# Kernel tuning notes

Measured on AMD Instinct MI355X. Metric: run time of the kernel, lower is better.

## Reference

```python
import jax, jax.numpy as jnp
import numpy as np

N, E = 100000, 1600000
IN_DIM, HID, NCLS = 64, 128, 18
BATCH, K = 8, 5000


def setup_inputs() -> dict:
    key = jax.random.key(0)
    ks = jax.random.split(key, 9)
    features = jax.random.normal(ks[0], (N, IN_DIM), dtype=jnp.float32)
    src = jax.random.randint(ks[1], (E,), 0, N, dtype=jnp.int32)
    dst = jax.random.randint(ks[2], (E,), 0, N, dtype=jnp.int32)
    def glorot(k, shape):
        lim = float(np.sqrt(6.0 / (shape[0] + shape[1])))
        return jax.random.uniform(k, shape, jnp.float32, -lim, lim)
    W1 = glorot(ks[3], (IN_DIM, HID)); b1 = jnp.zeros((HID,), jnp.float32)
    W2 = glorot(ks[4], (HID, HID));    b2 = jnp.zeros((HID,), jnp.float32)
    W3 = glorot(ks[5], (K * HID, NCLS)); b3 = jnp.zeros((NCLS,), jnp.float32)
    return {"features": features, "src": src, "dst": dst,
            "W1": W1, "b1": b1, "W2": W2, "b2": b2, "W3": W3, "b3": b3}


def reference(features, src, dst, W1, b1, W2, b2, W3, b3):
    n = features.shape[0]
    ones = jnp.ones(src.shape[0], features.dtype)
    out_deg = jax.ops.segment_sum(ones, src, num_segments=n)
    in_deg = jax.ops.segment_sum(ones, dst, num_segments=n)
    norm_src = jnp.clip(out_deg, 1.0) ** -0.5  # DGL norm='both'
    norm_dst = jnp.clip(in_deg, 1.0) ** -0.5

    def gconv(x, W, b, act):
        h = (x @ W) * norm_src[:, None]          # transform then normalize src
        agg = jax.ops.segment_sum(h[src], dst, num_segments=n)  # gather+scatter-add
        agg = agg * norm_dst[:, None] + b
        return jax.nn.relu(agg) if act else agg

    h = gconv(features, W1, b1, True)   # [N, HID]
    h = gconv(h, W2, b2, True)          # [N, HID]

    # global_sort_pool: equal-sized graphs of N//BATCH nodes, top-K by last channel
    n_per = n // BATCH
    hb = h.reshape(BATCH, n_per, HID)
    _, idx = jax.lax.top_k(hb[..., -1], K)                  # [B, K] descending
    topk = jnp.take_along_axis(hb, idx[..., None], axis=1)  # [B, K, HID]
    pooled = topk.reshape(BATCH, K * HID)

    return pooled @ W3 + b3  # [B, NCLS]
```

## Files before the change

### kernel.cpp

```cpp
#include <hip/hip_runtime.h>
#include <cstdint>
#include <cstddef>

#define N_NODES 100000
#define N_EDGES 1600000
#define IN_DIM  64
#define HID     128
#define NCLS    18
#define BATCH   8
#define TOPK    5000
#define NPER    12500
#define SORTN   16384
#define SORTC   2048

#define BSHIFT  9
#define BNODES  (1 << BSHIFT)
#define NBUCK   ((N_NODES + BNODES - 1) / BNODES)
#define CHUNK   8192


__global__ __launch_bounds__(256) void k_bcount(const int* __restrict__ src,
                                                const int* __restrict__ dst,
                                                int* __restrict__ bcntS,
                                                int* __restrict__ bcntD) {
    __shared__ int cs[NBUCK], cd[NBUCK];
    for (int b = threadIdx.x; b < NBUCK; b += 256) { cs[b] = 0; cd[b] = 0; }
    __syncthreads();
    const int base = blockIdx.x * CHUNK;
    const int end  = min(base + CHUNK, N_EDGES);
    for (int e = base + threadIdx.x; e < end; e += 256) {
        atomicAdd(&cs[src[e] >> BSHIFT], 1);
        atomicAdd(&cd[dst[e] >> BSHIFT], 1);
    }
    __syncthreads();
    for (int b = threadIdx.x; b < NBUCK; b += 256) {
        if (cs[b]) atomicAdd(&bcntS[b], cs[b]);
        if (cd[b]) atomicAdd(&bcntD[b], cd[b]);
    }
}

__global__ void k_bscan(const int* __restrict__ bcntS, const int* __restrict__ bcntD,
                        int* __restrict__ baseS, int* __restrict__ baseD,
                        int* __restrict__ curS, int* __restrict__ curD) {
    if (threadIdx.x == 0 && blockIdx.x == 0) {
        int rs = 0, rd = 0;
        for (int b = 0; b < NBUCK; ++b) {
            baseS[b] = rs; curS[b] = rs; rs += bcntS[b];
            baseD[b] = rd; curD[b] = rd; rd += bcntD[b];
        }
        baseS[NBUCK] = rs; baseD[NBUCK] = rd;
    }
}


__global__ __launch_bounds__(256) void k_bin(const int* __restrict__ src,
                                             const int* __restrict__ dst,
                                             int* __restrict__ cursorD,
                                             unsigned* __restrict__ binbuf) {
    __shared__ int cnt[NBUCK];
    __shared__ int gbase[NBUCK];
    __shared__ int cnt2[NBUCK];
    const int base = blockIdx.x * CHUNK;
    const int end  = min(base + CHUNK, N_EDGES);
    for (int b = threadIdx.x; b < NBUCK; b += 256) { cnt[b] = 0; cnt2[b] = 0; }
    __syncthreads();
    for (int e = base + threadIdx.x; e < end; e += 256)
        atomicAdd(&cnt[dst[e] >> BSHIFT], 1);
    __syncthreads();
    for (int b = threadIdx.x; b < NBUCK; b += 256)
        if (cnt[b] > 0) gbase[b] = atomicAdd(&cursorD[b], cnt[b]);
    __syncthreads();
    for (int e = base + threadIdx.x; e < end; e += 256) {
        int d = dst[e];
        int b = d >> BSHIFT;
        int off = atomicAdd(&cnt2[b], 1);
        unsigned packed = ((unsigned)(d & (BNODES - 1)) << 17) | (unsigned)src[e];
        binbuf[gbase[b] + off] = packed;
    }
}

__global__ __launch_bounds__(256) void k_bin_src(const int* __restrict__ src,
                                                 int* __restrict__ cursorS,
                                                 unsigned* __restrict__ sbin) {
    __shared__ int cnt[NBUCK];
    __shared__ int gbase[NBUCK];
    __shared__ int cnt2[NBUCK];
    const int base = blockIdx.x * CHUNK;
    const int end  = min(base + CHUNK, N_EDGES);
    for (int b = threadIdx.x; b < NBUCK; b += 256) { cnt[b] = 0; cnt2[b] = 0; }
    __syncthreads();
    for (int e = base + threadIdx.x; e < end; e += 256)
        atomicAdd(&cnt[src[e] >> BSHIFT], 1);
    __syncthreads();
    for (int b = threadIdx.x; b < NBUCK; b += 256)
        if (cnt[b] > 0) gbase[b] = atomicAdd(&cursorS[b], cnt[b]);
    __syncthreads();
    for (int e = base + threadIdx.x; e < end; e += 256) {
        int s = src[e];
        int b = s >> BSHIFT;
        int off = atomicAdd(&cnt2[b], 1);
        sbin[gbase[b] + off] = (unsigned)(s & (BNODES - 1));
    }
}


__global__ __launch_bounds__(256) void k_histS(const unsigned* __restrict__ sbin,
                                               const int* __restrict__ baseS,
                                               float* __restrict__ normS) {
    __shared__ int cnt[BNODES];
    for (int t = threadIdx.x; t < BNODES; t += 256) cnt[t] = 0;
    __syncthreads();
    const int beg = baseS[blockIdx.x], end = baseS[blockIdx.x + 1];
    for (int e = beg + threadIdx.x; e < end; e += 256)
        atomicAdd(&cnt[sbin[e]], 1);
    __syncthreads();
    const int nodeBase = blockIdx.x << BSHIFT;
    for (int t = threadIdx.x; t < BNODES; t += 256) {
        int node = nodeBase + t;
        if (node < N_NODES)
            normS[node] = 1.0f / sqrtf((float)max(cnt[t], 1));
    }
}

__global__ __launch_bounds__(256) void k_histD_scatter(const unsigned* __restrict__ binbuf,
                                                       const int* __restrict__ baseD,
                                                       float* __restrict__ normD,
                                                       int* __restrict__ row_ptr,
                                                       int* __restrict__ ssrc) {
    __shared__ int cnt[BNODES];
    __shared__ int tmp[BNODES];
    for (int t = threadIdx.x; t < BNODES; t += 256) cnt[t] = 0;
    __syncthreads();
    const int beg = baseD[blockIdx.x], end = baseD[blockIdx.x + 1];
    for (int e = beg + threadIdx.x; e < end; e += 256)
        atomicAdd(&cnt[binbuf[e] >> 17], 1);
    __syncthreads();
    const int nodeBase = blockIdx.x << BSHIFT;
    for (int t = threadIdx.x; t < BNODES; t += 256) {
        int node = nodeBase + t;
        if (node < N_NODES)
            normD[node] = 1.0f / sqrtf((float)max(cnt[t], 1));
    }
    for (int s = 1; s < BNODES; s <<= 1) {
        for (int t = threadIdx.x; t < BNODES; t += 256)
            tmp[t] = (t >= s) ? cnt[t - s] + cnt[t] : cnt[t];
        __syncthreads();
        for (int t = threadIdx.x; t < BNODES; t += 256) cnt[t] = tmp[t];
        __syncthreads();
    }
    for (int t = threadIdx.x; t < BNODES; t += 256) {
        int b = beg + ((t == 0) ? 0 : cnt[t - 1]);
        tmp[t] = b;
        int node = nodeBase + t;
        if (node < N_NODES) row_ptr[node] = b;
    }
    if (blockIdx.x == 0 && threadIdx.x == 0) row_ptr[N_NODES] = N_EDGES;
    __syncthreads();
    for (int e = beg + threadIdx.x; e < end; e += 256) {
        unsigned v = binbuf[e];
        int pos = atomicAdd(&tmp[v >> 17], 1);
        ssrc[pos] = (int)(v & 0x1FFFFu);
    }
}


#define BMT 64
#define BKT 32

template<int KDIM>
__global__ __launch_bounds__(256) void k_gemm_rt(const float* __restrict__ X,
                                                 const float* __restrict__ W,
                                                 const float* __restrict__ normS,
                                                 float* __restrict__ out) {
    __shared__ float xs[BMT][BKT + 4];
    __shared__ float ws[BKT * HID];

    const int tid = threadIdx.x;
    const int tx = tid & 31;
    const int ty = tid >> 5;
    const int col0 = tx * 4;
    const int row0 = ty * 8;
    const int rt = blockIdx.x * BMT;

    float acc[8][4];
    #pragma unroll
    for (int r = 0; r < 8; ++r)
        #pragma unroll
        for (int c = 0; c < 4; ++c) acc[r][c] = 0.f;

    for (int k0 = 0; k0 < KDIM; k0 += BKT) {
        __syncthreads();
        {
            const float4* wsrc = (const float4*)(W + (size_t)k0 * HID);
            #pragma unroll
            for (int i = tid; i < BKT * HID / 4; i += 256)
                ((float4*)ws)[i] = wsrc[i];
        }
        {
            #pragma unroll
            for (int i = tid; i < BMT * BKT / 4; i += 256) {
                int row = i >> 3;
                int kq  = i & 7;
                int gr  = rt + row;
                float4 v = make_float4(0.f, 0.f, 0.f, 0.f);
                if (gr < N_NODES)
                    v = *(const float4*)(X + (size_t)gr * KDIM + k0 + kq * 4);
                *(float4*)&xs[row][kq * 4] = v;
            }
        }
        __syncthreads();

        #pragma unroll 4
        for (int k = 0; k < BKT; ++k) {
            float4 b = *(const float4*)&ws[k * HID + col0];
            float a[8];
            #pragma unroll
            for (int r = 0; r < 8; ++r) a[r] = xs[row0 + r][k];
            #pragma unroll
            for (int r = 0; r < 8; ++r) {
                acc[r][0] += a[r] * b.x;
                acc[r][1] += a[r] * b.y;
                acc[r][2] += a[r] * b.z;
                acc[r][3] += a[r] * b.w;
            }
        }
    }

    #pragma unroll
    for (int r = 0; r < 8; ++r) {
        int gr = rt + row0 + r;
        if (gr < N_NODES) {
            float s = normS[gr];
            float4 o = make_float4(acc[r][0] * s, acc[r][1] * s, acc[r][2] * s, acc[r][3] * s);
            *(float4*)(out + (size_t)gr * HID + col0) = o;
        }
    }
}


#define ACC4(A, V) { A.x += V.x; A.y += V.y; A.z += V.z; A.w += V.w; }

__global__ __launch_bounds__(256) void k_agg(const float* __restrict__ hs,
                                             const int* __restrict__ row_ptr,
                                             const int* __restrict__ ssrc,
                                             const float* __restrict__ normD,
                                             const float* __restrict__ bias,
                                             float* __restrict__ out,
                                             float* __restrict__ keys) {
    const int node = blockIdx.x * 8 + (threadIdx.x >> 5);
    const int lane = threadIdx.x & 31;
    if (node >= N_NODES) return;
    const int beg = row_ptr[node], end = row_ptr[node + 1];
    const float4* __restrict__ hv = (const float4*)hs;
    float4 acc = make_float4(0.f, 0.f, 0.f, 0.f);
    int e = beg;
    for (; e + 8 <= end; e += 8) {
        int s0 = ssrc[e + 0], s1 = ssrc[e + 1], s2 = ssrc[e + 2], s3 = ssrc[e + 3];
        int s4 = ssrc[e + 4], s5 = ssrc[e + 5], s6 = ssrc[e + 6], s7 = ssrc[e + 7];
        float4 v0 = hv[(size_t)s0 * 32 + lane];
        float4 v1 = hv[(size_t)s1 * 32 + lane];
        float4 v2 = hv[(size_t)s2 * 32 + lane];
        float4 v3 = hv[(size_t)s3 * 32 + lane];
        float4 v4 = hv[(size_t)s4 * 32 + lane];
        float4 v5 = hv[(size_t)s5 * 32 + lane];
        float4 v6 = hv[(size_t)s6 * 32 + lane];
        float4 v7 = hv[(size_t)s7 * 32 + lane];
        ACC4(acc, v0); ACC4(acc, v1); ACC4(acc, v2); ACC4(acc, v3);
        ACC4(acc, v4); ACC4(acc, v5); ACC4(acc, v6); ACC4(acc, v7);
    }
    if (e + 4 <= end) {
        int s0 = ssrc[e + 0], s1 = ssrc[e + 1], s2 = ssrc[e + 2], s3 = ssrc[e + 3];
        float4 v0 = hv[(size_t)s0 * 32 + lane];
        float4 v1 = hv[(size_t)s1 * 32 + lane];
        float4 v2 = hv[(size_t)s2 * 32 + lane];
        float4 v3 = hv[(size_t)s3 * 32 + lane];
        ACC4(acc, v0); ACC4(acc, v1); ACC4(acc, v2); ACC4(acc, v3);
        e += 4;
    }
    for (; e < end; ++e) {
        float4 v0 = hv[(size_t)ssrc[e] * 32 + lane];
        ACC4(acc, v0);
    }
    float nrm = normD[node];
    float4 bb = *(const float4*)(bias + lane * 4);
    float4 o;
    o.x = fmaxf(acc.x * nrm + bb.x, 0.f);
    o.y = fmaxf(acc.y * nrm + bb.y, 0.f);
    o.z = fmaxf(acc.z * nrm + bb.z, 0.f);
    o.w = fmaxf(acc.w * nrm + bb.w, 0.f);
    *(float4*)(out + (size_t)node * HID + lane * 4) = o;
    if (keys != nullptr && lane == 31) keys[node] = o.w;
}


__global__ __launch_bounds__(256) void k_sort_init(const float* __restrict__ keys,
                                                   unsigned long long* __restrict__ arr) {
    int i = blockIdx.x * 256 + threadIdx.x;
    if (i >= BATCH * SORTN) return;
    int g = i >> 14;
    int l = i & (SORTN - 1);
    unsigned long long c;
    if (l < NPER) {
        unsigned u = __float_as_uint(keys[g * NPER + l]);
        unsigned s = (u & 0x80000000u) ? ~u : (u | 0x80000000u);
        unsigned d = ~s;
        c = ((unsigned long long)d << 32) | (unsigned)l;
    } else {
        c = 0xFFFFFFFFFFFFFFFFull;
    }
    arr[i] = c;
}

__global__ __launch_bounds__(1024) void k_sort_local_full(unsigned long long* __restrict__ arr) {
    __shared__ unsigned long long lds[SORTC];
    const int base  = blockIdx.x * SORTC;
    const int gbase = base & (SORTN - 1);
    lds[threadIdx.x]        = arr[base + threadIdx.x];
    lds[threadIdx.x + 1024] = arr[base + threadIdx.x + 1024];
    __syncthreads();
    for (int k = 2; k <= SORTC; k <<= 1) {
        for (int j = k >> 1; j > 0; j >>= 1) {
            int t = threadIdx.x;
            int i = ((t & ~(j - 1)) << 1) | (t & (j - 1));
            bool up = (((gbase + i) & k) == 0);
            unsigned long long a = lds[i], b = lds[i + j];
            if ((a > b) == up) { lds[i] = b; lds[i + j] = a; }
            __syncthreads();
        }
    }
    arr[base + threadIdx.x]        = lds[threadIdx.x];
    arr[base + threadIdx.x + 1024] = lds[threadIdx.x + 1024];
}

__global__ __launch_bounds__(256) void k_sort_global(unsigned long long* __restrict__ arr,
                                                     int k, int j) {
    int tg = blockIdx.x * 256 + threadIdx.x;
    if (tg >= BATCH * (SORTN / 2)) return;
    int g = tg >> 13;
    int t = tg & (SORTN / 2 - 1);
    int i = ((t & ~(j - 1)) << 1) | (t & (j - 1));
    bool up = ((i & k) == 0);
    unsigned long long* p = arr + (size_t)g * SORTN;
    unsigned long long a = p[i], b = p[i + j];
    if ((a > b) == up) { p[i] = b; p[i + j] = a; }
}

__global__ __launch_bounds__(1024) void k_sort_local_tail(unsigned long long* __restrict__ arr,
                                                          int k) {
    __shared__ unsigned long long lds[SORTC];
    const int base  = blockIdx.x * SORTC;
    const int gbase = base & (SORTN - 1);
    lds[threadIdx.x]        = arr[base + threadIdx.x];
    lds[threadIdx.x + 1024] = arr[base + threadIdx.x + 1024];
    __syncthreads();
    for (int j = SORTC >> 1; j > 0; j >>= 1) {
        int t = threadIdx.x;
        int i = ((t & ~(j - 1)) << 1) | (t & (j - 1));
        bool up = (((gbase + i) & k) == 0);
        unsigned long long a = lds[i], b = lds[i + j];
        if ((a > b) == up) { lds[i] = b; lds[i + j] = a; }
        __syncthreads();
    }
    arr[base + threadIdx.x]        = lds[threadIdx.x];
    arr[base + threadIdx.x + 1024] = lds[threadIdx.x + 1024];
}

__global__ __launch_bounds__(256) void k_sort_emit(const unsigned long long* __restrict__ arr,
                                                   int* __restrict__ topk_idx) {
    int i = blockIdx.x * 256 + threadIdx.x;
    if (i >= BATCH * TOPK) return;
    int b = i / TOPK;
    int k = i - b * TOPK;
    topk_idx[i] = (int)(arr[(size_t)b * SORTN + k] & 0xFFFFFFFFull);
}


__global__ void k_outinit(const float* __restrict__ b3, float* __restrict__ out) {
    int i = threadIdx.x;
    if (i < BATCH * NCLS) out[i] = b3[i % NCLS];
}

#define KPB 100

__global__ __launch_bounds__(128) void k_final(const float* __restrict__ h2,
                                               const int* __restrict__ topk_idx,
                                               const float* __restrict__ W3,
                                               float* __restrict__ out) {
    __shared__ float red[128 * NCLS];
    const int b = blockIdx.x / (TOPK / KPB);
    const int chunk = blockIdx.x % (TOPK / KPB);
    const int j = threadIdx.x;
    float acc[NCLS];
    #pragma unroll
    for (int c = 0; c < NCLS; ++c) acc[c] = 0.f;
    const int k0 = chunk * KPB;
    for (int k = k0; k < k0 + KPB; ++k) {
        int node = b * NPER + topk_idx[b * TOPK + k];
        float h = h2[(size_t)node * HID + j];
        const float* wrow = W3 + (size_t)(k * HID + j) * NCLS;
        #pragma unroll
        for (int c = 0; c < NCLS; ++c) acc[c] += h * wrow[c];
    }
    #pragma unroll
    for (int c = 0; c < NCLS; ++c) red[j * NCLS + c] = acc[c];
    __syncthreads();
    for (int s = 64; s > 0; s >>= 1) {
        if (j < s) {
            #pragma unroll
            for (int c = 0; c < NCLS; ++c) red[j * NCLS + c] += red[(j + s) * NCLS + c];
        }
        __syncthreads();
    }
    if (j < NCLS) atomicAdd(&out[b * NCLS + j], red[j]);
}


extern "C" void kernel_launch(void* const* d_in, const int* in_sizes, int n_in,
                              void* d_out, int out_size, void* d_ws, size_t ws_size,
                              hipStream_t stream) {
    const float* features = (const float*)d_in[0];
    const int*   src      = (const int*)d_in[1];
    const int*   dst      = (const int*)d_in[2];
    const float* W1       = (const float*)d_in[3];
    const float* b1       = (const float*)d_in[4];
    const float* W2       = (const float*)d_in[5];
    const float* b2       = (const float*)d_in[6];
    const float* W3       = (const float*)d_in[7];
    const float* b3       = (const float*)d_in[8];
    float* out = (float*)d_out;

    char* p = (char*)d_ws;
    auto carve = [&](size_t bytes) -> void* {
        void* r = (void*)p;
        p += (bytes + 511) & ~(size_t)511;
        return r;
    };
    float* normS     = (float*)carve((size_t)N_NODES * 4);
    float* normD     = (float*)carve((size_t)N_NODES * 4);
    int*   row_ptr   = (int*)carve((size_t)(N_NODES + 1) * 4);
    int*   bcntS     = (int*)carve((size_t)NBUCK * 4);
    int*   bcntD     = (int*)carve((size_t)NBUCK * 4);
    int*   baseS     = (int*)carve((size_t)(NBUCK + 1) * 4);
    int*   baseD     = (int*)carve((size_t)(NBUCK + 1) * 4);
    int*   curS      = (int*)carve((size_t)NBUCK * 4);
    int*   curD      = (int*)carve((size_t)NBUCK * 4);
    int*   ssrc      = (int*)carve((size_t)N_EDGES * 4);
    unsigned* binbuf = (unsigned*)carve((size_t)N_EDGES * 4);
    unsigned* sbin   = (unsigned*)carve((size_t)N_EDGES * 4);
    float* keys      = (float*)carve((size_t)N_NODES * 4);
    int*   topk_idx  = (int*)carve((size_t)BATCH * TOPK * 4);
    unsigned long long* sortbuf = (unsigned long long*)carve((size_t)BATCH * SORTN * 8);
    float* bufA      = (float*)carve((size_t)N_NODES * HID * 4);
    float* bufB      = (float*)carve((size_t)N_NODES * HID * 4);

    const int GB = (N_NODES + BMT - 1) / BMT;
    const int BB = (N_EDGES + CHUNK - 1) / CHUNK;

    hipMemsetAsync(bcntS, 0, (size_t)NBUCK * 4, stream);
    hipMemsetAsync(bcntD, 0, (size_t)NBUCK * 4, stream);

    k_bcount<<<BB, 256, 0, stream>>>(src, dst, bcntS, bcntD);
    k_bscan<<<1, 64, 0, stream>>>(bcntS, bcntD, baseS, baseD, curS, curD);
    k_bin<<<BB, 256, 0, stream>>>(src, dst, curD, binbuf);
    k_bin_src<<<BB, 256, 0, stream>>>(src, curS, sbin);
    k_histS<<<NBUCK, 256, 0, stream>>>(sbin, baseS, normS);
    k_histD_scatter<<<NBUCK, 256, 0, stream>>>(binbuf, baseD, normD, row_ptr, ssrc);

    k_gemm_rt<IN_DIM><<<GB, 256, 0, stream>>>(features, W1, normS, bufA);
    k_agg<<<(N_NODES + 7) / 8, 256, 0, stream>>>(bufA, row_ptr, ssrc, normD, b1, bufB, nullptr);
    k_gemm_rt<HID><<<GB, 256, 0, stream>>>(bufB, W2, normS, bufA);
    k_agg<<<(N_NODES + 7) / 8, 256, 0, stream>>>(bufA, row_ptr, ssrc, normD, b2, bufB, keys);

    const int NCHUNK = BATCH * SORTN / SORTC;
    const int GCE    = (BATCH * (SORTN / 2) + 255) / 256;
    k_sort_init<<<(BATCH * SORTN + 255) / 256, 256, 0, stream>>>(keys, sortbuf);
    k_sort_local_full<<<NCHUNK, 1024, 0, stream>>>(sortbuf);
    k_sort_global<<<GCE, 256, 0, stream>>>(sortbuf, 4096, 2048);
    k_sort_local_tail<<<NCHUNK, 1024, 0, stream>>>(sortbuf, 4096);
    k_sort_global<<<GCE, 256, 0, stream>>>(sortbuf, 8192, 4096);
    k_sort_global<<<GCE, 256, 0, stream>>>(sortbuf, 8192, 2048);
    k_sort_local_tail<<<NCHUNK, 1024, 0, stream>>>(sortbuf, 8192);
    k_sort_global<<<GCE, 256, 0, stream>>>(sortbuf, 16384, 8192);
    k_sort_global<<<GCE, 256, 0, stream>>>(sortbuf, 16384, 4096);
    k_sort_global<<<GCE, 256, 0, stream>>>(sortbuf, 16384, 2048);
    k_sort_local_tail<<<NCHUNK, 1024, 0, stream>>>(sortbuf, 16384);
    k_sort_emit<<<(BATCH * TOPK + 255) / 256, 256, 0, stream>>>(sortbuf, topk_idx);

    k_outinit<<<1, 256, 0, stream>>>(b3, out);
    k_final<<<BATCH * (TOPK / KPB), 128, 0, stream>>>(bufB, topk_idx, W3, out);
}
```

Baseline: 650.1 us.

## Aggregate before transform in first layer and fuse normalization/bias/ReLU into GEMM epilogue

Reorders the GCN layers as aggregate-then-transform. Layer 1 now gathers 64-wide input features, scaling each by the source norm, before the GEMM, which halves the gather traffic for that layer. The destination norm, bias, ReLU, next-layer source norm and top-k key extraction all move into the GEMM epilogue, so the aggregation kernels become plain gather-sums. The cost is an extra normS gather per edge in the first aggregation, a new 64-wide intermediate buffer, and a shorter unroll (4 instead of 8) in the 128-wide aggregation.

```diff
diff --git a/kernel.cpp b/kernel.cpp
--- a/kernel.cpp
+++ b/kernel.cpp
@@ -164,13 +164,78 @@
 }
 
 
+__global__ __launch_bounds__(256) void k_agg64(const float* __restrict__ hs,
+                                               const int* __restrict__ row_ptr,
+                                               const int* __restrict__ ssrc,
+                                               const float* __restrict__ normS,
+                                               float* __restrict__ out) {
+    const int node = blockIdx.x * 16 + (threadIdx.x >> 4);
+    const int lane = threadIdx.x & 15;
+    if (node >= N_NODES) return;
+    const int beg = row_ptr[node], end = row_ptr[node + 1];
+    const float4* __restrict__ hv = (const float4*)hs;
+    float4 acc = make_float4(0.f, 0.f, 0.f, 0.f);
+    int e = beg;
+    for (; e + 4 <= end; e += 4) {
+        int s0 = ssrc[e + 0], s1 = ssrc[e + 1], s2 = ssrc[e + 2], s3 = ssrc[e + 3];
+        float n0 = normS[s0], n1 = normS[s1], n2 = normS[s2], n3 = normS[s3];
+        float4 v0 = hv[(size_t)s0 * 16 + lane];
+        float4 v1 = hv[(size_t)s1 * 16 + lane];
+        float4 v2 = hv[(size_t)s2 * 16 + lane];
+        float4 v3 = hv[(size_t)s3 * 16 + lane];
+        acc.x += v0.x * n0; acc.y += v0.y * n0; acc.z += v0.z * n0; acc.w += v0.w * n0;
+        acc.x += v1.x * n1; acc.y += v1.y * n1; acc.z += v1.z * n1; acc.w += v1.w * n1;
+        acc.x += v2.x * n2; acc.y += v2.y * n2; acc.z += v2.z * n2; acc.w += v2.w * n2;
+        acc.x += v3.x * n3; acc.y += v3.y * n3; acc.z += v3.z * n3; acc.w += v3.w * n3;
+    }
+    for (; e < end; ++e) {
+        int s0 = ssrc[e];
+        float n0 = normS[s0];
+        float4 v0 = hv[(size_t)s0 * 16 + lane];
+        acc.x += v0.x * n0; acc.y += v0.y * n0; acc.z += v0.z * n0; acc.w += v0.w * n0;
+    }
+    *(float4*)(out + (size_t)node * IN_DIM + lane * 4) = acc;
+}
+
+#define ACC4(A, V) { A.x += V.x; A.y += V.y; A.z += V.z; A.w += V.w; }
+
+__global__ __launch_bounds__(256) void k_agg128(const float* __restrict__ hs,
+                                                const int* __restrict__ row_ptr,
+                                                const int* __restrict__ ssrc,
+                                                float* __restrict__ out) {
+    const int node = blockIdx.x * 8 + (threadIdx.x >> 5);
+    const int lane = threadIdx.x & 31;
+    if (node >= N_NODES) return;
+    const int beg = row_ptr[node], end = row_ptr[node + 1];
+    const float4* __restrict__ hv = (const float4*)hs;
+    float4 acc = make_float4(0.f, 0.f, 0.f, 0.f);
+    int e = beg;
+    for (; e + 4 <= end; e += 4) {
+        int s0 = ssrc[e + 0], s1 = ssrc[e + 1], s2 = ssrc[e + 2], s3 = ssrc[e + 3];
+        float4 v0 = hv[(size_t)s0 * 32 + lane];
+        float4 v1 = hv[(size_t)s1 * 32 + lane];
+        float4 v2 = hv[(size_t)s2 * 32 + lane];
+        float4 v3 = hv[(size_t)s3 * 32 + lane];
+        ACC4(acc, v0); ACC4(acc, v1); ACC4(acc, v2); ACC4(acc, v3);
+    }
+    for (; e < end; ++e) {
+        float4 v0 = hv[(size_t)ssrc[e] * 32 + lane];
+        ACC4(acc, v0);
+    }
+    *(float4*)(out + (size_t)node * HID + lane * 4) = acc;
+}
+
+
 #define BMT 64
 #define BKT 32
 
-template<int KDIM>
+template<int KDIM, bool POST, bool KEYS>
 __global__ __launch_bounds__(256) void k_gemm_rt(const float* __restrict__ X,
                                                  const float* __restrict__ W,
+                                                 const float* __restrict__ normD,
+                                                 const float* __restrict__ bias,
                                                  const float* __restrict__ normS,
+                                                 float* __restrict__ keys,
                                                  float* __restrict__ out) {
     __shared__ float xs[BMT][BKT + 4];
     __shared__ float ws[BKT * HID];
@@ -226,70 +291,25 @@
         }
     }
 
+    const float4 bb = *(const float4*)(bias + col0);
     #pragma unroll
     for (int r = 0; r < 8; ++r) {
         int gr = rt + row0 + r;
         if (gr < N_NODES) {
-            float s = normS[gr];
-            float4 o = make_float4(acc[r][0] * s, acc[r][1] * s, acc[r][2] * s, acc[r][3] * s);
+            float nd = normD[gr];
+            float4 o;
+            o.x = fmaxf(acc[r][0] * nd + bb.x, 0.f);
+            o.y = fmaxf(acc[r][1] * nd + bb.y, 0.f);
+            o.z = fmaxf(acc[r][2] * nd + bb.z, 0.f);
+            o.w = fmaxf(acc[r][3] * nd + bb.w, 0.f);
+            if (KEYS && col0 == 124) keys[gr] = o.w;
+            if (POST) {
+                float ns = normS[gr];
+                o.x *= ns; o.y *= ns; o.z *= ns; o.w *= ns;
+            }
             *(float4*)(out + (size_t)gr * HID + col0) = o;
         }
     }
-}
-
-
-#define ACC4(A, V) { A.x += V.x; A.y += V.y; A.z += V.z; A.w += V.w; }
-
-__global__ __launch_bounds__(256) void k_agg(const float* __restrict__ hs,
-                                             const int* __restrict__ row_ptr,
-                                             const int* __restrict__ ssrc,
-                                             const float* __restrict__ normD,
-                                             const float* __restrict__ bias,
-                                             float* __restrict__ out,
-                                             float* __restrict__ keys) {
-    const int node = blockIdx.x * 8 + (threadIdx.x >> 5);
-    const int lane = threadIdx.x & 31;
-    if (node >= N_NODES) return;
-    const int beg = row_ptr[node], end = row_ptr[node + 1];
-    const float4* __restrict__ hv = (const float4*)hs;
-    float4 acc = make_float4(0.f, 0.f, 0.f, 0.f);
-    int e = beg;
-    for (; e + 8 <= end; e += 8) {
-        int s0 = ssrc[e + 0], s1 = ssrc[e + 1], s2 = ssrc[e + 2], s3 = ssrc[e + 3];
-        int s4 = ssrc[e + 4], s5 = ssrc[e + 5], s6 = ssrc[e + 6], s7 = ssrc[e + 7];
-        float4 v0 = hv[(size_t)s0 * 32 + lane];
-        float4 v1 = hv[(size_t)s1 * 32 + lane];
-        float4 v2 = hv[(size_t)s2 * 32 + lane];
-        float4 v3 = hv[(size_t)s3 * 32 + lane];
-        float4 v4 = hv[(size_t)s4 * 32 + lane];
-        float4 v5 = hv[(size_t)s5 * 32 + lane];
-        float4 v6 = hv[(size_t)s6 * 32 + lane];
-        float4 v7 = hv[(size_t)s7 * 32 + lane];
-        ACC4(acc, v0); ACC4(acc, v1); ACC4(acc, v2); ACC4(acc, v3);
-        ACC4(acc, v4); ACC4(acc, v5); ACC4(acc, v6); ACC4(acc, v7);
-    }
-    if (e + 4 <= end) {
-        int s0 = ssrc[e + 0], s1 = ssrc[e + 1], s2 = ssrc[e + 2], s3 = ssrc[e + 3];
-        float4 v0 = hv[(size_t)s0 * 32 + lane];
-        float4 v1 = hv[(size_t)s1 * 32 + lane];
-        float4 v2 = hv[(size_t)s2 * 32 + lane];
-        float4 v3 = hv[(size_t)s3 * 32 + lane];
-        ACC4(acc, v0); ACC4(acc, v1); ACC4(acc, v2); ACC4(acc, v3);
-        e += 4;
-    }
-    for (; e < end; ++e) {
-        float4 v0 = hv[(size_t)ssrc[e] * 32 + lane];
-        ACC4(acc, v0);
-    }
-    float nrm = normD[node];
-    float4 bb = *(const float4*)(bias + lane * 4);
-    float4 o;
-    o.x = fmaxf(acc.x * nrm + bb.x, 0.f);
-    o.y = fmaxf(acc.y * nrm + bb.y, 0.f);
-    o.z = fmaxf(acc.z * nrm + bb.z, 0.f);
-    o.w = fmaxf(acc.w * nrm + bb.w, 0.f);
-    *(float4*)(out + (size_t)node * HID + lane * 4) = o;
-    if (keys != nullptr && lane == 31) keys[node] = o.w;
 }
 
 
@@ -452,6 +472,7 @@
     unsigned long long* sortbuf = (unsigned long long*)carve((size_t)BATCH * SORTN * 8);
     float* bufA      = (float*)carve((size_t)N_NODES * HID * 4);
     float* bufB      = (float*)carve((size_t)N_NODES * HID * 4);
+    float* g1        = (float*)carve((size_t)N_NODES * IN_DIM * 4);
 
     const int GB = (N_NODES + BMT - 1) / BMT;
     const int BB = (N_EDGES + CHUNK - 1) / CHUNK;
@@ -466,10 +487,10 @@
     k_histS<<<NBUCK, 256, 0, stream>>>(sbin, baseS, normS);
     k_histD_scatter<<<NBUCK, 256, 0, stream>>>(binbuf, baseD, normD, row_ptr, ssrc);
 
-    k_gemm_rt<IN_DIM><<<GB, 256, 0, stream>>>(features, W1, normS, bufA);
-    k_agg<<<(N_NODES + 7) / 8, 256, 0, stream>>>(bufA, row_ptr, ssrc, normD, b1, bufB, nullptr);
-    k_gemm_rt<HID><<<GB, 256, 0, stream>>>(bufB, W2, normS, bufA);
-    k_agg<<<(N_NODES + 7) / 8, 256, 0, stream>>>(bufA, row_ptr, ssrc, normD, b2, bufB, keys);
+    k_agg64<<<(N_NODES + 15) / 16, 256, 0, stream>>>(features, row_ptr, ssrc, normS, g1);
+    k_gemm_rt<IN_DIM, true, false><<<GB, 256, 0, stream>>>(g1, W1, normD, b1, normS, nullptr, bufA);
+    k_agg128<<<(N_NODES + 7) / 8, 256, 0, stream>>>(bufA, row_ptr, ssrc, bufB);
+    k_gemm_rt<HID, false, true><<<GB, 256, 0, stream>>>(bufB, W2, normD, b2, nullptr, keys, bufA);
 
     const int NCHUNK = BATCH * SORTN / SORTC;
     const int GCE    = (BATCH * (SORTN / 2) + 255) / 256;
@@ -487,5 +508,5 @@
     k_sort_emit<<<(BATCH * TOPK + 255) / 256, 256, 0, stream>>>(sortbuf, topk_idx);
 
     k_outinit<<<1, 256, 0, stream>>>(b3, out);
-    k_final<<<BATCH * (TOPK / KPB), 128, 0, stream>>>(bufB, topk_idx, W3, out);
-}
+    k_final<<<BATCH * (TOPK / KPB), 128, 0, stream>>>(bufA, topk_idx, W3, out);
+}
```

Measured after the change: 594.7 us. 1.09x faster.
